# Performance work log

Hardware: AMD Instinct MI355X
Metric: run time of the kernel (lower is better)

## Reference

```python
import jax, jax.numpy as jnp
import numpy as np

N = 10000      # nodes
E = 160000     # edges
F_IN = 84
H = 256
P = 4          # powers [0,1,2,3]
L = 3          # mixhop layers


def setup_inputs() -> dict:
    key = jax.random.key(0)
    ks = jax.random.split(key, 10)
    s = 0.05
    inp = {}
    inp["x"] = jax.random.normal(ks[0], (N, F_IN), jnp.float32)
    inp["edge_index"] = jax.random.randint(ks[1], (2, E), 0, N, dtype=jnp.int32)
    inp["w_in"] = jax.random.normal(ks[2], (F_IN, H), jnp.float32) * s
    inp["b_in"] = jnp.zeros((H,), jnp.float32)
    inp["mh_w0"] = jax.random.normal(ks[3], (P, H, H), jnp.float32) * s
    inp["mh_b0"] = jnp.zeros((P, H), jnp.float32)
    inp["mh_w12"] = jax.random.normal(ks[4], (2, P, P * H, H), jnp.float32) * s
    inp["mh_b12"] = jnp.zeros((2, P, H), jnp.float32)
    inp["ln_g"] = jnp.ones((L, P * H), jnp.float32)
    inp["ln_b"] = jnp.zeros((L, P * H), jnp.float32)
    inp["w1"] = jax.random.normal(ks[5], (P * H, H), jnp.float32) * s
    inp["b1"] = jnp.zeros((H,), jnp.float32)
    inp["w2"] = jax.random.normal(ks[6], (H, H // 2), jnp.float32) * s
    inp["b2"] = jnp.zeros((H // 2,), jnp.float32)
    inp["w3"] = jax.random.normal(ks[7], (H // 2, 1), jnp.float32) * s
    inp["b3"] = jnp.zeros((1,), jnp.float32)
    return inp


def _gcn_norm(edge_index, n):
    # D^{-1/2} (A + I) D^{-1/2}, PyG gcn_norm with add_self_loops=True
    loop = jnp.arange(n, dtype=edge_index.dtype)
    src = jnp.concatenate([edge_index[0], loop])
    dst = jnp.concatenate([edge_index[1], loop])
    deg = jax.ops.segment_sum(jnp.ones(src.shape[0], jnp.float32), dst, num_segments=n)
    dinv = jnp.where(deg > 0, deg ** -0.5, 0.0)
    return src, dst, dinv[src] * dinv[dst]


def _propagate(h, src, dst, w, n):
    # out[i] = sum_{(j->i)} w_e * h[j]
    return jax.ops.segment_sum(h[src] * w[:, None], dst, num_segments=n)


def _mixhop(h, src, dst, w, n, W, B):
    outs = [h @ W[0] + B[0]]  # power 0
    for p in range(1, W.shape[0]):
        h = _propagate(h, src, dst, w, n)
        outs.append(h @ W[p] + B[p])
    return jnp.concatenate(outs, axis=-1)  # [n, P*H]


def _layernorm(x, g, b, eps=1e-5):
    mu = x.mean(-1, keepdims=True)
    var = x.var(-1, keepdims=True)
    return (x - mu) * jax.lax.rsqrt(var + eps) * g + b


def reference(x, edge_index, w_in, b_in, mh_w0, mh_b0, mh_w12, mh_b12,
              ln_g, ln_b, w1, b1, w2, b2, w3, b3):
    gelu = lambda t: jax.nn.gelu(t, approximate=False)  # torch default (erf)
    n = x.shape[0]
    src, dst, w = _gcn_norm(edge_index, n)
    h = gelu(x @ w_in + b_in)
    for i in range(L):
        W, B = (mh_w0, mh_b0) if i == 0 else (mh_w12[i - 1], mh_b12[i - 1])
        h = _mixhop(h, src, dst, w, n, W, B)
        h = gelu(_layernorm(h, ln_g[i], ln_b[i]))
        # dropout inactive at inference
    h = gelu(h @ w1 + b1)
    h = gelu(h @ w2 + b2)
    out = h @ w3 + b3
    return out.squeeze(-1)  # [N]
```

## Files before the change

kernel.cpp:

```cpp
#include <hip/hip_runtime.h>

typedef unsigned short u16;
typedef unsigned int u32;
typedef __bf16 bf16x8 __attribute__((ext_vector_type(8)));
typedef float f32x4 __attribute__((ext_vector_type(4)));

#define NN 10000
#define EE 160000
#define MPAD 10112

__device__ inline float b2f(u16 u) { return __uint_as_float(((u32)u) << 16); }
__device__ inline u16 f2b(float f) {
    u32 u = __float_as_uint(f);
    return (u16)((u + 0x7fffu + ((u >> 16) & 1u)) >> 16);
}
__device__ inline float gelu_f(float x) {
    return 0.5f * x * (1.0f + erff(x * 0.70710678118654752f));
}
__device__ inline void load_lds16(const u16* g, u16* l) {
    __builtin_amdgcn_global_load_lds((const __attribute__((address_space(1))) u32*)g,
                                     (__attribute__((address_space(3))) u32*)l, 16, 0, 0);
}

__global__ __launch_bounds__(256) void k_count(const int* __restrict__ dst, int* __restrict__ cnt) {
    int e = blockIdx.x * 256 + threadIdx.x;
    if (e < EE) atomicAdd(&cnt[dst[e]], 1);
}

__global__ __launch_bounds__(256) void k_scan(const int* __restrict__ cnt, int* __restrict__ rowptr,
                                              int* __restrict__ cursor, float* __restrict__ dinv) {
    __shared__ int part[256];
    const int t = threadIdx.x;
    const int CH = 40;
    int base = t * CH;
    int ssum = 0;
    for (int k = 0; k < CH; k++) { int i = base + k; if (i < NN) ssum += cnt[i]; }
    part[t] = ssum;
    __syncthreads();
    for (int off = 1; off < 256; off <<= 1) {
        int v = (t >= off) ? part[t - off] : 0;
        __syncthreads();
        part[t] += v;
        __syncthreads();
    }
    int run = part[t] - ssum;
    for (int k = 0; k < CH; k++) {
        int i = base + k;
        if (i < NN) {
            rowptr[i] = run; cursor[i] = run;
            int c = cnt[i];
            dinv[i] = rsqrtf((float)(c + 1));
            run += c;
        }
    }
    if (t == 255) rowptr[NN] = run;
}

__global__ __launch_bounds__(256) void k_fill(const int* __restrict__ src, const int* __restrict__ dst,
                                              int* __restrict__ cursor, int* __restrict__ cols,
                                              float* __restrict__ vals, const float* __restrict__ dinv) {
    int e = blockIdx.x * 256 + threadIdx.x;
    if (e < EE) {
        int s = src[e], d = dst[e];
        int pos = atomicAdd(&cursor[d], 1);
        cols[pos] = s;
        vals[pos] = dinv[s] * dinv[d];
    }
}

__global__ __launch_bounds__(256) void k_padx(const float* __restrict__ x, u16* __restrict__ xp) {
    int idx = blockIdx.x * 256 + threadIdx.x;
    if (idx >= MPAD * 128) return;
    int r = idx >> 7, c = idx & 127;
    u16 v = 0;
    if (r < NN && c < 84) v = f2b(x[(size_t)r * 84 + c]);
    xp[idx] = v;
}

struct TT { const float* src; u16* dst; int K, Nc, Kp; };
__global__ __launch_bounds__(256) void k_transT(TT t0, TT t1, TT t2, TT t3, TT t4) {
    int b = blockIdx.x; TT T;
    if (b < 8)        { T = t0; }
    else if (b < 72)  { T = t1; b -= 8; }
    else if (b < 584) { T = t2; b -= 72; }
    else if (b < 648) { T = t3; b -= 584; }
    else              { T = t4; b -= 648; }
    int tk = (T.Kp + 63) >> 6, tn = T.Nc >> 6;
    int bb  = b / (tk * tn);
    int rem = b - bb * (tk * tn);
    int k0 = (rem / tn) * 64, n0 = (rem % tn) * 64;
    __shared__ u16 tile[64][65];
    const float* src = T.src + (size_t)bb * T.K * T.Nc;
    u16* dst = T.dst + (size_t)bb * T.Nc * T.Kp;
    int c = threadIdx.x & 63, r0 = threadIdx.x >> 6;
#pragma unroll
    for (int i = 0; i < 16; i++) {
        int r = r0 + i * 4;
        int k = k0 + r;
        u16 v = 0;
        if (k < T.K) v = f2b(src[(size_t)k * T.Nc + n0 + c]);
        tile[r][c] = v;
    }
    __syncthreads();
    int rr = threadIdx.x & 63, cc0 = threadIdx.x >> 6;
#pragma unroll
    for (int i = 0; i < 16; i++) {
        int cc = cc0 + i * 4;
        int k = k0 + rr;
        if (k < T.Kp) dst[(size_t)(n0 + cc) * T.Kp + k] = tile[rr][cc];
    }
}

struct CvtSrcs { const float *b_in, *mh_b0, *mh_b12, *ln_g, *ln_b, *b1, *b2, *w3, *b3; };
__global__ __launch_bounds__(256) void k_cvt_all(CvtSrcs S, u16* __restrict__ dst) {
    int i = blockIdx.x * 256 + threadIdx.x;
    const float* s; int base;
    if (i < 256)       { s = S.b_in;   base = 0; }
    else if (i < 1280) { s = S.mh_b0;  base = 256; }
    else if (i < 3328) { s = S.mh_b12; base = 1280; }
    else if (i < 6400) { s = S.ln_g;   base = 3328; }
    else if (i < 9472) { s = S.ln_b;   base = 6400; }
    else if (i < 9728) { s = S.b1;     base = 9472; }
    else if (i < 9856) { s = S.b2;     base = 9728; }
    else if (i < 9984) { s = S.w3;     base = 9856; }
    else if (i < 9985) { s = S.b3;     base = 9984; }
    else return;
    dst[i] = f2b(s[i - base]);
}

template<int TM, int TN, int ACT, int EPI, int BATCH>
__global__ __launch_bounds__(256) void k_gemm(const u16* __restrict__ A0, const u16* __restrict__ A1,
                                              const u16* __restrict__ A2, const u16* __restrict__ A3,
                                              const u16* __restrict__ Bt, const u16* __restrict__ bias,
                                              u16* __restrict__ C, u16* __restrict__ Z,
                                              int K, int ldc, int col0, int NB_M, int NB_N) {
    constexpr int AM = TM / 32, AN = TN / 32;
    constexpr int CA = TM / 16, CB = TN / 16;
    constexpr int NCH = (CA + CB) / 4;
    constexpr int SLOT = (TM + TN) * 32;
    __shared__ __align__(16) u16 Sh[4][SLOT];
    int id = blockIdx.x;
    int g8 = id & 7, sIdx = id >> 3;
    int nb = sIdx % NB_N, jb = sIdx / NB_N;
    int mb = g8 + 8 * jb;
    if (mb >= NB_M) return;
    const u16* A = A0;
    if (BATCH) {
        int z = blockIdx.y;
        if (z == 1) A = A1; else if (z == 2) A = A2; else if (z == 3) A = A3;
        Bt   += (size_t)z * 256 * K;
        bias += z * 256;
        col0 += z * 256;
    }
    const int t = threadIdx.x;
    const int wv = t >> 6, lane = t & 63;
    const int wm = wv >> 1, wn = wv & 1;
    const int quad = lane >> 4, l16 = lane & 15;
    const int tileM = mb * TM, tileN = nb * TN;

    f32x4 acc[AM][AN] = {};

    const int rch = lane >> 2, c8 = (lane & 3) * 8;
    const u16* gsrc[NCH];
    int lofs[NCH];
#pragma unroll
    for (int i = 0; i < NCH; i++) {
        int c = wv + 4 * i;
        if (c < CA) {
            gsrc[i] = A + (size_t)(tileM + c * 16 + rch) * K + c8;
            lofs[i] = c * 512 + lane * 8;
        } else {
            int cc = c - CA;
            gsrc[i] = Bt + (size_t)(tileN + cc * 16 + rch) * K + c8;
            lofs[i] = TM * 32 + cc * 512 + lane * 8;
        }
    }

#pragma unroll
    for (int i = 0; i < NCH; i++) load_lds16(gsrc[i], &Sh[0][lofs[i]]);
#pragma unroll
    for (int i = 0; i < NCH; i++) load_lds16(gsrc[i] + 32, &Sh[1][lofs[i]]);

    const int npair = K >> 6;
    for (int p = 0; p < npair; p++) {
        __syncthreads();
        int cur = (p & 1) << 1;
        int nxt = cur ^ 2;
        int kc = p << 6;
        if (kc + 64 < K) {
#pragma unroll
            for (int i = 0; i < NCH; i++) load_lds16(gsrc[i] + kc + 64, &Sh[nxt][lofs[i]]);
#pragma unroll
            for (int i = 0; i < NCH; i++) load_lds16(gsrc[i] + kc + 96, &Sh[nxt + 1][lofs[i]]);
        }
#pragma unroll
        for (int h = 0; h < 2; h++) {
            const u16* S = Sh[cur + h];
            bf16x8 af[AM], bfr[AN];
#pragma unroll
            for (int tm = 0; tm < AM; tm++)
                af[tm] = *(const bf16x8*)&S[(wm * (TM / 2) + tm * 16 + l16) * 32 + quad * 8];
#pragma unroll
            for (int tn = 0; tn < AN; tn++)
                bfr[tn] = *(const bf16x8*)&S[TM * 32 + (wn * (TN / 2) + tn * 16 + l16) * 32 + quad * 8];
#pragma unroll
            for (int tm = 0; tm < AM; tm++)
#pragma unroll
                for (int tn = 0; tn < AN; tn++)
                    acc[tm][tn] = __builtin_amdgcn_mfma_f32_16x16x32_bf16(af[tm], bfr[tn], acc[tm][tn], 0, 0, 0);
        }
    }

#pragma unroll
    for (int tm = 0; tm < AM; tm++)
#pragma unroll
        for (int tn = 0; tn < AN; tn++)
#pragma unroll
            for (int r = 0; r < 4; r++) {
                int row = tileM + wm * (TM / 2) + tm * 16 + quad * 4 + r;
                int col = tileN + wn * (TN / 2) + tn * 16 + l16;
                float v = acc[tm][tn][r];
                if (EPI == 2) {
                    if (col < 256) C[(size_t)row * 1024 + col] = f2b(v + b2f(bias[col]));
                    else           Z[(size_t)row * 768 + (col - 256)] = f2b(v);
                } else {
                    v += b2f(bias[col]);
                    if (ACT) v = gelu_f(v);
                    C[(size_t)row * ldc + col0 + col] = f2b(v);
                }
            }
}

template<int CAT0>
__global__ __launch_bounds__(256) void k_propw(const u16* __restrict__ hin, int W, int G,
                                               const int* __restrict__ rowptr, const int* __restrict__ cols,
                                               const float* __restrict__ vals, const float* __restrict__ dinv,
                                               u16* __restrict__ concat, const u16* __restrict__ bias,
                                               int col0, u16* __restrict__ out2) {
    int unit = blockIdx.x * 4 + (threadIdx.x >> 6);
    if (unit >= NN * G) return;
    int g = unit / NN, node = unit - g * NN;
    int lane = threadIdx.x & 63;
    int half = lane >> 5, fl = lane & 31;
    const u16* base = hin + g * 256 + fl * 8;
    float a0 = 0, a1 = 0, a2 = 0, a3 = 0, a4 = 0, a5 = 0, a6 = 0, a7 = 0;
    if (half == 1) {
        float di = dinv[node], sw = di * di;
        bf16x8 sv = *(const bf16x8*)(base + (size_t)node * W);
        a0 = sw * (float)sv[0]; a1 = sw * (float)sv[1]; a2 = sw * (float)sv[2]; a3 = sw * (float)sv[3];
        a4 = sw * (float)sv[4]; a5 = sw * (float)sv[5]; a6 = sw * (float)sv[6]; a7 = sw * (float)sv[7];
    }
    int s = rowptr[node], e = rowptr[node + 1];
    int q = s + half;
    for (; q + 6 < e; q += 8) {
        int j0 = cols[q], j1 = cols[q + 2], j2 = cols[q + 4], j3 = cols[q + 6];
        float w0 = vals[q], w1 = vals[q + 2], w2 = vals[q + 4], w3 = vals[q + 6];
        bf16x8 v0 = *(const bf16x8*)(base + (size_t)j0 * W);
        bf16x8 v1 = *(const bf16x8*)(base + (size_t)j1 * W);
        bf16x8 v2 = *(const bf16x8*)(base + (size_t)j2 * W);
        bf16x8 v3 = *(const bf16x8*)(base + (size_t)j3 * W);
        a0 += w0 * (float)v0[0] + w1 * (float)v1[0] + w2 * (float)v2[0] + w3 * (float)v3[0];
        a1 += w0 * (float)v0[1] + w1 * (float)v1[1] + w2 * (float)v2[1] + w3 * (float)v3[1];
        a2 += w0 * (float)v0[2] + w1 * (float)v1[2] + w2 * (float)v2[2] + w3 * (float)v3[2];
        a3 += w0 * (float)v0[3] + w1 * (float)v1[3] + w2 * (float)v2[3] + w3 * (float)v3[3];
        a4 += w0 * (float)v0[4] + w1 * (float)v1[4] + w2 * (float)v2[4] + w3 * (float)v3[4];
        a5 += w0 * (float)v0[5] + w1 * (float)v1[5] + w2 * (float)v2[5] + w3 * (float)v3[5];
        a6 += w0 * (float)v0[6] + w1 * (float)v1[6] + w2 * (float)v2[6] + w3 * (float)v3[6];
        a7 += w0 * (float)v0[7] + w1 * (float)v1[7] + w2 * (float)v2[7] + w3 * (float)v3[7];
    }
    for (; q + 2 < e; q += 4) {
        int j0 = cols[q], j1 = cols[q + 2];
        float w0 = vals[q], w1 = vals[q + 2];
        bf16x8 v0 = *(const bf16x8*)(base + (size_t)j0 * W);
        bf16x8 v1 = *(const bf16x8*)(base + (size_t)j1 * W);
        a0 += w0 * (float)v0[0] + w1 * (float)v1[0];
        a1 += w0 * (float)v0[1] + w1 * (float)v1[1];
        a2 += w0 * (float)v0[2] + w1 * (float)v1[2];
        a3 += w0 * (float)v0[3] + w1 * (float)v1[3];
        a4 += w0 * (float)v0[4] + w1 * (float)v1[4];
        a5 += w0 * (float)v0[5] + w1 * (float)v1[5];
        a6 += w0 * (float)v0[6] + w1 * (float)v1[6];
        a7 += w0 * (float)v0[7] + w1 * (float)v1[7];
    }
    if (q < e) {
        int j = cols[q];
        float w = vals[q];
        bf16x8 v = *(const bf16x8*)(base + (size_t)j * W);
        a0 += w * (float)v[0]; a1 += w * (float)v[1]; a2 += w * (float)v[2]; a3 += w * (float)v[3];
        a4 += w * (float)v[4]; a5 += w * (float)v[5]; a6 += w * (float)v[6]; a7 += w * (float)v[7];
    }
    a0 += __shfl_down(a0, 32); a1 += __shfl_down(a1, 32);
    a2 += __shfl_down(a2, 32); a3 += __shfl_down(a3, 32);
    a4 += __shfl_down(a4, 32); a5 += __shfl_down(a5, 32);
    a6 += __shfl_down(a6, 32); a7 += __shfl_down(a7, 32);
    if (half == 0) {
        int f = fl * 8;
        union { u16 u[8]; uint4 v; } pk;
        if (CAT0 && g == 0) {
            pk.u[0] = f2b(a0 + b2f(bias[f + 0])); pk.u[1] = f2b(a1 + b2f(bias[f + 1]));
            pk.u[2] = f2b(a2 + b2f(bias[f + 2])); pk.u[3] = f2b(a3 + b2f(bias[f + 3]));
            pk.u[4] = f2b(a4 + b2f(bias[f + 4])); pk.u[5] = f2b(a5 + b2f(bias[f + 5]));
            pk.u[6] = f2b(a6 + b2f(bias[f + 6])); pk.u[7] = f2b(a7 + b2f(bias[f + 7]));
            *(uint4*)(concat + (size_t)node * 1024 + col0 + f) = pk.v;
        } else {
            int W2 = W - CAT0 * 256;
            pk.u[0] = f2b(a0); pk.u[1] = f2b(a1); pk.u[2] = f2b(a2); pk.u[3] = f2b(a3);
            pk.u[4] = f2b(a4); pk.u[5] = f2b(a5); pk.u[6] = f2b(a6); pk.u[7] = f2b(a7);
            *(uint4*)(out2 + (size_t)node * W2 + (g - CAT0) * 256 + f) = pk.v;
        }
    }
}

__global__ __launch_bounds__(256) void k_ln_gelu(const u16* __restrict__ X, const u16* __restrict__ g,
                                                 const u16* __restrict__ b, u16* __restrict__ out) {
    __shared__ float red[256];
    const int row = blockIdx.x, t = threadIdx.x;
    ushort4 xv = *(const ushort4*)(X + (size_t)row * 1024 + t * 4);
    float x0 = b2f(xv.x), x1 = b2f(xv.y), x2 = b2f(xv.z), x3 = b2f(xv.w);
    red[t] = x0 + x1 + x2 + x3;
    __syncthreads();
    for (int off = 128; off; off >>= 1) {
        if (t < off) red[t] += red[t + off];
        __syncthreads();
    }
    float mu = red[0] * (1.f / 1024.f);
    __syncthreads();
    float d0 = x0 - mu, d1 = x1 - mu, d2 = x2 - mu, d3 = x3 - mu;
    red[t] = d0 * d0 + d1 * d1 + d2 * d2 + d3 * d3;
    __syncthreads();
    for (int off = 128; off; off >>= 1) {
        if (t < off) red[t] += red[t + off];
        __syncthreads();
    }
    float rs = rsqrtf(red[0] * (1.f / 1024.f) + 1e-5f);
    int c = t * 4;
    ushort4 gv = *(const ushort4*)(g + c);
    ushort4 bv = *(const ushort4*)(b + c);
    ushort4 o;
    o.x = f2b(gelu_f(d0 * rs * b2f(gv.x) + b2f(bv.x)));
    o.y = f2b(gelu_f(d1 * rs * b2f(gv.y) + b2f(bv.y)));
    o.z = f2b(gelu_f(d2 * rs * b2f(gv.z) + b2f(bv.z)));
    o.w = f2b(gelu_f(d3 * rs * b2f(gv.w) + b2f(bv.w)));
    *(ushort4*)(out + (size_t)row * 1024 + c) = o;
}

__global__ __launch_bounds__(256) void k_final(const u16* __restrict__ h, const u16* __restrict__ w3,
                                               const u16* __restrict__ b3, float* __restrict__ out) {
    int gw = (blockIdx.x * 256 + threadIdx.x) >> 6;
    int lane = threadIdx.x & 63;
    if (gw >= NN) return;
    u32 hv = *(const u32*)(h + (size_t)gw * 128 + lane * 2);
    u32 wv = *(const u32*)(w3 + lane * 2);
    float s = b2f((u16)(hv & 0xffff)) * b2f((u16)(wv & 0xffff)) +
              b2f((u16)(hv >> 16)) * b2f((u16)(wv >> 16));
    for (int off = 32; off; off >>= 1) s += __shfl_down(s, off);
    if (lane == 0) out[gw] = s + b2f(b3[0]);
}

extern "C" void kernel_launch(void* const* d_in, const int* in_sizes, int n_in,
                              void* d_out, int out_size, void* d_ws, size_t ws_size,
                              hipStream_t stream) {
    (void)in_sizes; (void)n_in; (void)out_size; (void)ws_size;
    const float* x  = (const float*)d_in[0];
    const int*   ei = (const int*)d_in[1];
    float* out = (float*)d_out;

    char* p = (char*)d_ws;
    auto alloc = [&](size_t bytes) { char* q = p; p += (bytes + 255) & ~(size_t)255; return q; };
    int*   cnt    = (int*)alloc(NN * 4);
    int*   rowptr = (int*)alloc((NN + 1) * 4);
    int*   cursor = (int*)alloc(NN * 4);
    float* dinv   = (float*)alloc(NN * 4);
    int*   cols   = (int*)alloc(EE * 4);
    float* vals   = (float*)alloc(EE * 4);
    u16*   xp     = (u16*)alloc((size_t)MPAD * 128 * 2);
    u16*   wbuf   = (u16*)alloc((size_t)2686976 * 2);
    u16*   smallC = (u16*)alloc(10240 * 2);
    u16*   S1     = (u16*)alloc((size_t)MPAD * 256 * 2);
    u16*   S2     = (u16*)alloc((size_t)MPAD * 256 * 2);
    u16*   S3     = (u16*)alloc((size_t)MPAD * 256 * 2);
    u16*   S4     = (u16*)alloc((size_t)MPAD * 256 * 2);
    u16*   Zb     = (u16*)alloc((size_t)MPAD * 768 * 2);
    u16*   Y2     = (u16*)alloc((size_t)MPAD * 512 * 2);
    u16*   Y3     = (u16*)alloc((size_t)MPAD * 256 * 2);
    u16*   bufA   = (u16*)alloc((size_t)MPAD * 1024 * 2);
    u16*   concat = (u16*)alloc((size_t)MPAD * 1024 * 2);

    u16* winT  = wbuf;
    u16* w0T   = wbuf + 32768;
    u16* w12T  = wbuf + 294912;
    u16* w1T   = wbuf + 2392064;
    u16* w2T   = wbuf + 2654208;
    u16* binC  = smallC;
    u16* mb0C  = smallC + 256;
    u16* mb12C = smallC + 1280;
    u16* lngC  = smallC + 3328;
    u16* lnbC  = smallC + 6400;
    u16* b1C   = smallC + 9472;
    u16* b2C   = smallC + 9728;
    u16* w3C   = smallC + 9856;
    u16* b3C   = smallC + 9984;

    const int* srcA = ei;
    const int* dstA = ei + EE;

    hipMemsetAsync(cnt, 0, NN * 4, stream);

    k_padx<<<(MPAD * 128 + 255) / 256, 256, 0, stream>>>(x, xp);
    TT t0{(const float*)d_in[2],  winT, 84,   256, 128};
    TT t1{(const float*)d_in[4],  w0T,  256,  256, 256};
    TT t2{(const float*)d_in[6],  w12T, 1024, 256, 1024};
    TT t3{(const float*)d_in[10], w1T,  1024, 256, 1024};
    TT t4{(const float*)d_in[12], w2T,  256,  128, 256};
    k_transT<<<656, 256, 0, stream>>>(t0, t1, t2, t3, t4);
    CvtSrcs CS{(const float*)d_in[3], (const float*)d_in[5], (const float*)d_in[7],
               (const float*)d_in[8], (const float*)d_in[9], (const float*)d_in[11],
               (const float*)d_in[13], (const float*)d_in[14], (const float*)d_in[15]};
    k_cvt_all<<<40, 256, 0, stream>>>(CS, smallC);

    k_count<<<(EE + 255) / 256, 256, 0, stream>>>(dstA, cnt);
    k_scan<<<1, 256, 0, stream>>>(cnt, rowptr, cursor, dinv);
    k_fill<<<(EE + 255) / 256, 256, 0, stream>>>(srcA, dstA, cursor, cols, vals, dinv);

    auto gx = [](int nbm, int nbn) { return 8 * ((nbm + 7) / 8) * nbn; };

    k_gemm<128, 64, 1, 0, 0><<<gx(79, 4), 256, 0, stream>>>(xp, xp, xp, xp, winT, binC, S1, nullptr, 128, 256, 0, 79, 4);

    k_propw<0><<<2500, 256, 0, stream>>>(S1, 256, 1, rowptr, cols, vals, dinv, nullptr, nullptr, 0, S2);
    k_propw<0><<<2500, 256, 0, stream>>>(S2, 256, 1, rowptr, cols, vals, dinv, nullptr, nullptr, 0, S3);
    k_propw<0><<<2500, 256, 0, stream>>>(S3, 256, 1, rowptr, cols, vals, dinv, nullptr, nullptr, 0, S4);
    k_gemm<128, 64, 0, 0, 1><<<dim3(gx(79, 4), 4), 256, 0, stream>>>(S1, S2, S3, S4, w0T, mb0C, concat, nullptr, 256, 1024, 0, 79, 4);
    k_ln_gelu<<<NN, 256, 0, stream>>>(concat, lngC, lnbC, bufA);

    for (int L = 0; L < 2; L++) {
        const u16* WT = w12T + (size_t)L * 1024 * 1024;
        const u16* BB = mb12C + L * 1024;
        k_gemm<128, 64, 0, 2, 0><<<gx(79, 16), 256, 0, stream>>>(bufA, bufA, bufA, bufA, WT, BB, concat, Zb, 1024, 0, 0, 79, 16);
        k_propw<1><<<7500, 256, 0, stream>>>(Zb, 768, 3, rowptr, cols, vals, dinv, concat, BB + 256, 256, Y2);
        k_propw<1><<<5000, 256, 0, stream>>>(Y2, 512, 2, rowptr, cols, vals, dinv, concat, BB + 512, 512, Y3);
        k_propw<1><<<2500, 256, 0, stream>>>(Y3, 256, 1, rowptr, cols, vals, dinv, concat, BB + 768, 768, Y3);
        k_ln_gelu<<<NN, 256, 0, stream>>>(concat, lngC + (L + 1) * 1024, lnbC + (L + 1) * 1024, bufA);
    }

    k_gemm<64, 64, 1, 0, 0><<<gx(158, 4), 256, 0, stream>>>(bufA, bufA, bufA, bufA, w1T, b1C, S1, nullptr, 1024, 256, 0, 158, 4);
    k_gemm<64, 64, 1, 0, 0><<<gx(158, 2), 256, 0, stream>>>(S1, S1, S1, S1, w2T, b2C, S2, nullptr, 256, 128, 0, 158, 2);
    k_final<<<2500, 256, 0, stream>>>(S2, w3C, b3C, out);
}
```

Measured before the change: 479.9 us.

## Load GEMM B operand directly into registers and widen tile shapes

The GEMM kernel no longer stages the transposed weight (B) tile through LDS. Each wave now loads its B fragments straight from global memory into registers, double-buffered one K-step ahead, while A keeps the async LDS path. Tile shapes change alongside: the input GEMM moves to 64x64 and the mixhop GEMMs to 128x128. This cuts LDS traffic and shared memory use and gives more reuse per block, at the cost of extra registers and uncoalesced, redundant global B reads across the M-waves.

Measured after the change: 556.2 us. 1.16x slower.

```diff
diff --git a/kernel.cpp b/kernel.cpp
--- a/kernel.cpp
+++ b/kernel.cpp
@@ -135,9 +135,9 @@
                                               u16* __restrict__ C, u16* __restrict__ Z,
                                               int K, int ldc, int col0, int NB_M, int NB_N) {
     constexpr int AM = TM / 32, AN = TN / 32;
-    constexpr int CA = TM / 16, CB = TN / 16;
-    constexpr int NCH = (CA + CB) / 4;
-    constexpr int SLOT = (TM + TN) * 32;
+    constexpr int CA = TM / 16;
+    constexpr int NCH = CA / 4;
+    constexpr int SLOT = TM * 32;
     __shared__ __align__(16) u16 Sh[4][SLOT];
     int id = blockIdx.x;
     int g8 = id & 7, sIdx = id >> 3;
@@ -166,20 +166,24 @@
 #pragma unroll
     for (int i = 0; i < NCH; i++) {
         int c = wv + 4 * i;
-        if (c < CA) {
-            gsrc[i] = A + (size_t)(tileM + c * 16 + rch) * K + c8;
-            lofs[i] = c * 512 + lane * 8;
-        } else {
-            int cc = c - CA;
-            gsrc[i] = Bt + (size_t)(tileN + cc * 16 + rch) * K + c8;
-            lofs[i] = TM * 32 + cc * 512 + lane * 8;
-        }
-    }
+        gsrc[i] = A + (size_t)(tileM + c * 16 + rch) * K + c8;
+        lofs[i] = c * 512 + lane * 8;
+    }
+    const u16* bb[AN];
+#pragma unroll
+    for (int tn = 0; tn < AN; tn++)
+        bb[tn] = Bt + (size_t)(tileN + wn * (TN / 2) + tn * 16 + l16) * K + quad * 8;
 
 #pragma unroll
     for (int i = 0; i < NCH; i++) load_lds16(gsrc[i], &Sh[0][lofs[i]]);
 #pragma unroll
     for (int i = 0; i < NCH; i++) load_lds16(gsrc[i] + 32, &Sh[1][lofs[i]]);
+    bf16x8 bc[2][AN], bn[2][AN];
+#pragma unroll
+    for (int h = 0; h < 2; h++)
+#pragma unroll
+        for (int tn = 0; tn < AN; tn++)
+            bc[h][tn] = *(const bf16x8*)(bb[tn] + h * 32);
 
     const int npair = K >> 6;
     for (int p = 0; p < npair; p++) {
@@ -192,22 +196,31 @@
             for (int i = 0; i < NCH; i++) load_lds16(gsrc[i] + kc + 64, &Sh[nxt][lofs[i]]);
 #pragma unroll
             for (int i = 0; i < NCH; i++) load_lds16(gsrc[i] + kc + 96, &Sh[nxt + 1][lofs[i]]);
+#pragma unroll
+            for (int h = 0; h < 2; h++)
+#pragma unroll
+                for (int tn = 0; tn < AN; tn++)
+                    bn[h][tn] = *(const bf16x8*)(bb[tn] + kc + 64 + h * 32);
         }
 #pragma unroll
         for (int h = 0; h < 2; h++) {
             const u16* S = Sh[cur + h];
-            bf16x8 af[AM], bfr[AN];
+            bf16x8 af[AM];
 #pragma unroll
             for (int tm = 0; tm < AM; tm++)
                 af[tm] = *(const bf16x8*)&S[(wm * (TM / 2) + tm * 16 + l16) * 32 + quad * 8];
 #pragma unroll
-            for (int tn = 0; tn < AN; tn++)
-                bfr[tn] = *(const bf16x8*)&S[TM * 32 + (wn * (TN / 2) + tn * 16 + l16) * 32 + quad * 8];
-#pragma unroll
             for (int tm = 0; tm < AM; tm++)
 #pragma unroll
                 for (int tn = 0; tn < AN; tn++)
-                    acc[tm][tn] = __builtin_amdgcn_mfma_f32_16x16x32_bf16(af[tm], bfr[tn], acc[tm][tn], 0, 0, 0);
+                    acc[tm][tn] = __builtin_amdgcn_mfma_f32_16x16x32_bf16(af[tm], bc[h][tn], acc[tm][tn], 0, 0, 0);
+        }
+        if (kc + 64 < K) {
+#pragma unroll
+            for (int h = 0; h < 2; h++)
+#pragma unroll
+                for (int tn = 0; tn < AN; tn++)
+                    bc[h][tn] = bn[h][tn];
         }
     }
 
@@ -424,18 +437,18 @@
 
     auto gx = [](int nbm, int nbn) { return 8 * ((nbm + 7) / 8) * nbn; };
 
-    k_gemm<128, 64, 1, 0, 0><<<gx(79, 4), 256, 0, stream>>>(xp, xp, xp, xp, winT, binC, S1, nullptr, 128, 256, 0, 79, 4);
+    k_gemm<64, 64, 1, 0, 0><<<gx(158, 4), 256, 0, stream>>>(xp, xp, xp, xp, winT, binC, S1, nullptr, 128, 256, 0, 158, 4);
 
     k_propw<0><<<2500, 256, 0, stream>>>(S1, 256, 1, rowptr, cols, vals, dinv, nullptr, nullptr, 0, S2);
     k_propw<0><<<2500, 256, 0, stream>>>(S2, 256, 1, rowptr, cols, vals, dinv, nullptr, nullptr, 0, S3);
     k_propw<0><<<2500, 256, 0, stream>>>(S3, 256, 1, rowptr, cols, vals, dinv, nullptr, nullptr, 0, S4);
-    k_gemm<128, 64, 0, 0, 1><<<dim3(gx(79, 4), 4), 256, 0, stream>>>(S1, S2, S3, S4, w0T, mb0C, concat, nullptr, 256, 1024, 0, 79, 4);
+    k_gemm<128, 128, 0, 0, 1><<<dim3(gx(79, 2), 4), 256, 0, stream>>>(S1, S2, S3, S4, w0T, mb0C, concat, nullptr, 256, 1024, 0, 79, 2);
     k_ln_gelu<<<NN, 256, 0, stream>>>(concat, lngC, lnbC, bufA);
 
     for (int L = 0; L < 2; L++) {
         const u16* WT = w12T + (size_t)L * 1024 * 1024;
         const u16* BB = mb12C + L * 1024;
-        k_gemm<128, 64, 0, 2, 0><<<gx(79, 16), 256, 0, stream>>>(bufA, bufA, bufA, bufA, WT, BB, concat, Zb, 1024, 0, 0, 79, 16);
+        k_gemm<128, 128, 0, 2, 0><<<gx(79, 8), 256, 0, stream>>>(bufA, bufA, bufA, bufA, WT, BB, concat, Zb, 1024, 0, 0, 79, 8);
         k_propw<1><<<7500, 256, 0, stream>>>(Zb, 768, 3, rowptr, cols, vals, dinv, concat, BB + 256, 256, Y2);
         k_propw<1><<<5000, 256, 0, stream>>>(Y2, 512, 2, rowptr, cols, vals, dinv, concat, BB + 512, 512, Y3);
         k_propw<1><<<2500, 256, 0, stream>>>(Y3, 256, 1, rowptr, cols, vals, dinv, concat, BB + 768, 768, Y3);
```
